# Performance work log

Measured on AMD Instinct MI355X. Metric: run time of the kernel, lower is better.

## Reference

```python
import jax, jax.numpy as jnp
import numpy as np

TOP_K = 2

def setup_inputs() -> dict:
    key = jax.random.key(0)
    ks = jax.random.split(key, 5)
    B, T, C, D, E = 2, 2048, 1024, 4096, 8
    init = 0.02  # typical GPT init scale
    return {
        "x": jax.random.normal(ks[0], (B, T, C), dtype=jnp.float32),
        "w_router": jax.random.normal(ks[1], (E, C), dtype=jnp.float32) * init,
        "w1": jax.random.normal(ks[2], (E, C, D), dtype=jnp.float32) * init,
        "b1": jnp.zeros((E, D), dtype=jnp.float32),
        "w2": jax.random.normal(ks[3], (E, D, C), dtype=jnp.float32) * init,
        "b2": jnp.zeros((E, C), dtype=jnp.float32),
    }

def reference(x, w_router, w1, b1, w2, b2):
    # Eval-mode MoE forward: no router noise, aux_loss = 0.
    B, T, C = x.shape
    E = w_router.shape[0]
    xf = x.reshape(B * T, C)                                   # [N, C]
    N = xf.shape[0]

    # Router: softmax over experts, top-2, renormalize.
    logits = jnp.einsum('nc,ec->ne', xf, w_router)             # [N, E]
    probs = jax.nn.softmax(logits, axis=-1)
    topw, topi = jax.lax.top_k(probs, TOP_K)                   # [N, K]
    topw = topw / jnp.sum(topw, axis=-1, keepdims=True)

    # Dense combine-weight matrix (scatter of top-k weights), zeros elsewhere.
    wdense = jnp.zeros((N, E), dtype=xf.dtype)
    wdense = wdense.at[jnp.arange(N)[:, None], topi].set(topw)  # [N, E]

    # Per-expert MLP (exact GELU, like torch nn.GELU default).
    h = jax.nn.gelu(jnp.einsum('nc,ecd->ned', xf, w1) + b1[None, :, :],
                    approximate=False)                          # [N, E, D]
    expert_out = jnp.einsum('ned,edc->nec', h, w2) + b2[None, :, :]  # [N, E, C]

    # Weighted scatter-combine: unselected experts have weight 0.
    out = jnp.einsum('ne,nec->nc', wdense, expert_out)          # [N, C]
    return out.reshape(B, T, C)
```

## Files before the change

### kernel.cpp

```cpp
#include <hip/hip_runtime.h>
#include <cstdint>

#define NTOK 4096
#define CDIM 1024
#define DDIM 4096
#define NEXP 8
#define PAIR_CAP 9216
#define MAXTILE 72

typedef __bf16 bf16x8 __attribute__((ext_vector_type(8)));
typedef float f32x4 __attribute__((ext_vector_type(4)));
typedef unsigned int u32x4 __attribute__((ext_vector_type(4)));
typedef unsigned short u16;

__device__ __forceinline__ u16 bf16_rne(float f) {
  unsigned u = __builtin_bit_cast(unsigned, f);
  u += 0x7fffu + ((u >> 16) & 1u);
  return (u16)(u >> 16);
}
__device__ __forceinline__ unsigned pk2(float a, float b) {
  return (unsigned)bf16_rne(a) | ((unsigned)bf16_rne(b) << 16);
}
__device__ __forceinline__ float bf2f(u16 v) {
  unsigned u = (unsigned)v << 16;
  return __builtin_bit_cast(float, u);
}
__device__ __forceinline__ bf16x8 ldfrag(const u16* p) {
  u32x4 v = *(const u32x4*)p;
  return __builtin_bit_cast(bf16x8, v);
}

typedef __attribute__((address_space(1))) const unsigned int as1_u32;
typedef __attribute__((address_space(3))) unsigned int as3_u32;
__device__ __forceinline__ void gload_lds16(const void* g, void* l) {
  __builtin_amdgcn_global_load_lds((as1_u32*)g, (as3_u32*)l, 16, 0, 0);
}

__global__ void k_router(const float* __restrict__ x, const float* __restrict__ wr,
                         int2* __restrict__ topi, float2* __restrict__ topw) {
  int n = blockIdx.x;
  int lane = threadIdx.x;
  const float* xr = x + (size_t)n * CDIM;
  float acc[NEXP];
#pragma unroll
  for (int e = 0; e < NEXP; ++e) acc[e] = 0.f;
  for (int c = lane; c < CDIM; c += 64) {
    float xv = xr[c];
#pragma unroll
    for (int e = 0; e < NEXP; ++e) acc[e] += xv * wr[e * CDIM + c];
  }
#pragma unroll
  for (int e = 0; e < NEXP; ++e) {
    float v = acc[e];
#pragma unroll
    for (int off = 32; off > 0; off >>= 1) v += __shfl_xor(v, off, 64);
    acc[e] = v;
  }
  if (lane == 0) {
    int i1 = 0; float l1 = acc[0];
#pragma unroll
    for (int e = 1; e < NEXP; ++e) if (acc[e] > l1) { l1 = acc[e]; i1 = e; }
    int i2 = (i1 == 0) ? 1 : 0; float l2 = acc[i2];
#pragma unroll
    for (int e = 0; e < NEXP; ++e)
      if (e != i1 && acc[e] > l2) { l2 = acc[e]; i2 = e; }
    float wa = 1.f / (1.f + expf(l2 - l1));
    topi[n] = make_int2(i1, i2);
    topw[n] = make_float2(wa, 1.f - wa);
  }
}

__global__ void k_count(const int2* __restrict__ topi, int* __restrict__ counts) {
  int n = blockIdx.x * blockDim.x + threadIdx.x;
  if (n < NTOK) {
    int2 tv = topi[n];
    atomicAdd(&counts[tv.x], 1);
    atomicAdd(&counts[tv.y], 1);
  }
}

__global__ void k_scan(const int* __restrict__ counts, int* __restrict__ poff,
                       int* __restrict__ cursor, int* __restrict__ ntiles,
                       int* __restrict__ tile_e, int* __restrict__ tile_base) {
  if (threadIdx.x == 0 && blockIdx.x == 0) {
    int o = 0, nt = 0;
    for (int e = 0; e < NEXP; ++e) {
      poff[e] = o;
      cursor[e] = o;
      int cap = (counts[e] + 127) & ~127;
      for (int tb = 0; tb < cap; tb += 128) { tile_e[nt] = e; tile_base[nt] = o + tb; ++nt; }
      o += cap;
    }
    poff[NEXP] = o;
    *ntiles = nt;
  }
}

__global__ void k_scatter(const int2* __restrict__ topi,
                          int* __restrict__ cursor, int* __restrict__ ptok,
                          int2* __restrict__ ppos) {
  int n = blockIdx.x * blockDim.x + threadIdx.x;
  if (n < NTOK) {
    int2 tv = topi[n];
    int p0 = atomicAdd(&cursor[tv.x], 1); ptok[p0] = n;
    int p1 = atomicAdd(&cursor[tv.y], 1); ptok[p1] = n;
    ppos[n] = make_int2(p0, p1);
  }
}

__global__ void k_xcast(const float* __restrict__ x, u16* __restrict__ xb) {
  int i = blockIdx.x * blockDim.x + threadIdx.x;
  float4 v = ((const float4*)x)[i];
  ushort4 o;
  o.x = bf16_rne(v.x); o.y = bf16_rne(v.y); o.z = bf16_rne(v.z); o.w = bf16_rne(v.w);
  ((ushort4*)xb)[i] = o;
}

__global__ __launch_bounds__(256) void k_transpose(const float* __restrict__ in,
                                                   u16* __restrict__ out, int K, int N) {
  __shared__ float tile[64][65];
  int e = blockIdx.z;
  int nb = blockIdx.x * 64, kb = blockIdx.y * 64;
  const float* src = in + (size_t)e * K * N + (size_t)kb * N + nb;
  int t = threadIdx.x;
#pragma unroll
  for (int j = 0; j < 4; ++j) {
    int idx4 = t + j * 256;
    int r = idx4 >> 4, c4 = idx4 & 15;
    float4 v = *(const float4*)&src[(size_t)r * N + c4 * 4];
    tile[r][c4 * 4 + 0] = v.x; tile[r][c4 * 4 + 1] = v.y;
    tile[r][c4 * 4 + 2] = v.z; tile[r][c4 * 4 + 3] = v.w;
  }
  __syncthreads();
  u16* dst = out + (size_t)e * N * K + (size_t)nb * K + kb;
#pragma unroll
  for (int j = 0; j < 8; ++j) {
    int idxp = t + j * 256;
    int n = idxp >> 5, kp = idxp & 31;
    unsigned pr = pk2(tile[kp * 2][n], tile[kp * 2 + 1][n]);
    *(unsigned*)&dst[(size_t)n * K + kp * 2] = pr;
  }
}

template <int KD, int NOUT, bool GATHER, bool DOGELU>
__global__ __launch_bounds__(256) void k_gemm(
    const u16* __restrict__ A, const u16* __restrict__ WT,
    const float* __restrict__ bias, const int* __restrict__ ntiles,
    const int* __restrict__ tile_e, const int* __restrict__ tile_base,
    const int* __restrict__ ptok, u16* __restrict__ Out) {
  int bx = blockIdx.x;
  if (bx >= *ntiles) return;
  int e = tile_e[bx];
  int pairbase = tile_base[bx];
  int colbase = blockIdx.y * 128;

  __shared__ __align__(16) u16 As[128 * 64];
  __shared__ __align__(16) u16 Bs[128 * 64];

  int t = threadIdx.x;
  int wid = t >> 6, lane = t & 63;
  int quad = lane >> 4, lm = lane & 15, l7 = lane & 7;
  int wm = wid & 1, wn = wid >> 1;
  int rl = lane >> 3, q = lane & 7;
  int kbl = (q - rl) & 7;

  const char* Ac = (const char*)A;
  const char* Wc = (const char*)WT;
  uint64_t gA[4], gB[4];
#pragma unroll
  for (int i = 0; i < 4; ++i) {
    int row = wid * 32 + i * 8 + rl;
    int arow = GATHER ? ptok[pairbase + row] : (pairbase + row);
    gA[i] = (uint64_t)arow * (KD * 2) + (uint64_t)kbl * 16;
    int brow = colbase + row;
    gB[i] = ((uint64_t)e * NOUT + brow) * (KD * 2) + (uint64_t)kbl * 16;
  }

  f32x4 acc[4][4];
  f32x4 zed = {0.f, 0.f, 0.f, 0.f};
#pragma unroll
  for (int a = 0; a < 4; ++a)
#pragma unroll
    for (int b = 0; b < 4; ++b) acc[a][b] = zed;

  for (int step = 0; step < KD / 64; ++step) {
    __syncthreads();
#pragma unroll
    for (int i = 0; i < 4; ++i)
      gload_lds16(Ac + gA[i] + (uint64_t)step * 128, (void*)&As[(wid * 32 + i * 8) * 64]);
#pragma unroll
    for (int i = 0; i < 4; ++i)
      gload_lds16(Wc + gB[i] + (uint64_t)step * 128, (void*)&Bs[(wid * 32 + i * 8) * 64]);
    __syncthreads();

#pragma unroll
    for (int s = 0; s < 2; ++s) {
      bf16x8 af[4], bfr[4];
#pragma unroll
      for (int tm = 0; tm < 4; ++tm) {
        int row = wm * 64 + tm * 16 + lm;
        int phys = (s * 4 + quad + l7) & 7;
        af[tm] = ldfrag(&As[row * 64 + phys * 8]);
      }
#pragma unroll
      for (int tn = 0; tn < 4; ++tn) {
        int col = wn * 64 + tn * 16 + lm;
        int phys = (s * 4 + quad + l7) & 7;
        bfr[tn] = ldfrag(&Bs[col * 64 + phys * 8]);
      }
#pragma unroll
      for (int tm = 0; tm < 4; ++tm)
#pragma unroll
        for (int tn = 0; tn < 4; ++tn)
          acc[tm][tn] = __builtin_amdgcn_mfma_f32_16x16x32_bf16(af[tm], bfr[tn], acc[tm][tn], 0, 0, 0);
    }
  }

#pragma unroll
  for (int tn = 0; tn < 4; ++tn) {
    int col = colbase + wn * 64 + tn * 16 + lm;
    float bv = bias[e * NOUT + col];
#pragma unroll
    for (int tm = 0; tm < 4; ++tm) {
      int row0 = pairbase + wm * 64 + tm * 16 + quad * 4;
#pragma unroll
      for (int i = 0; i < 4; ++i) {
        float vv = acc[tm][tn][i] + bv;
        if (DOGELU) vv = 0.5f * vv * (1.f + erff(vv * 0.70710678118654752f));
        Out[(size_t)(row0 + i) * NOUT + col] = bf16_rne(vv);
      }
    }
  }
}

__global__ __launch_bounds__(256) void k_combine(const u16* __restrict__ pairout,
                                                 const float2* __restrict__ topw,
                                                 const int2* __restrict__ ppos,
                                                 float* __restrict__ out) {
  int n = blockIdx.x, t = threadIdx.x;
  int2 p = ppos[n];
  float2 w = topw[n];
  ushort4 a = ((const ushort4*)(pairout + (size_t)p.x * CDIM))[t];
  ushort4 b = ((const ushort4*)(pairout + (size_t)p.y * CDIM))[t];
  float4 o;
  o.x = w.x * bf2f(a.x) + w.y * bf2f(b.x);
  o.y = w.x * bf2f(a.y) + w.y * bf2f(b.y);
  o.z = w.x * bf2f(a.z) + w.y * bf2f(b.z);
  o.w = w.x * bf2f(a.w) + w.y * bf2f(b.w);
  ((float4*)(out + (size_t)n * CDIM))[t] = o;
}

extern "C" void kernel_launch(void* const* d_in, const int* in_sizes, int n_in,
                              void* d_out, int out_size, void* d_ws, size_t ws_size,
                              hipStream_t stream) {
  const float* x  = (const float*)d_in[0];
  const float* wr = (const float*)d_in[1];
  const float* w1 = (const float*)d_in[2];
  const float* b1 = (const float*)d_in[3];
  const float* w2 = (const float*)d_in[4];
  const float* b2 = (const float*)d_in[5];
  float* out = (float*)d_out;
  char* ws = (char*)d_ws;

  int*    counts  = (int*)(ws + 0);
  int*    poff    = (int*)(ws + 64);
  int*    cursor  = (int*)(ws + 128);
  int*    ntiles  = (int*)(ws + 192);
  int*    tile_e  = (int*)(ws + 256);
  int*    tile_b  = (int*)(ws + 640);
  int2*   topi    = (int2*)(ws + 1024);
  float2* topw    = (float2*)(ws + 33792);
  int2*   ppos    = (int2*)(ws + 66560);
  int*    ptok    = (int*)(ws + 99328);
  u16*    xb      = (u16*)(ws + 136192);
  u16*    h       = (u16*)(ws + 8524800);
  u16*    wt      = (u16*)(ws + 84022272);
  u16*    pairout = (u16*)(ws + 151131136);

  hipMemsetAsync(ws, 0, 1024, stream);
  hipMemsetAsync(ws + 99328, 0, 36864, stream);

  k_router<<<NTOK, 64, 0, stream>>>(x, wr, topi, topw);
  k_count<<<NTOK / 256, 256, 0, stream>>>(topi, counts);
  k_scan<<<1, 64, 0, stream>>>(counts, poff, cursor, ntiles, tile_e, tile_b);
  k_scatter<<<NTOK / 256, 256, 0, stream>>>(topi, cursor, ptok, ppos);
  k_xcast<<<NTOK * CDIM / 4 / 256, 256, 0, stream>>>(x, xb);

  k_transpose<<<dim3(DDIM / 64, CDIM / 64, NEXP), 256, 0, stream>>>(w1, wt, CDIM, DDIM);
  k_gemm<CDIM, DDIM, true, true>
      <<<dim3(MAXTILE, DDIM / 128), 256, 0, stream>>>(xb, wt, b1, ntiles, tile_e, tile_b, ptok, h);

  k_transpose<<<dim3(CDIM / 64, DDIM / 64, NEXP), 256, 0, stream>>>(w2, wt, DDIM, CDIM);
  k_gemm<DDIM, CDIM, false, false>
      <<<dim3(MAXTILE, CDIM / 128), 256, 0, stream>>>(h, wt, b2, ntiles, tile_e, tile_b, ptok, pairout);

  k_combine<<<NTOK, 256, 0, stream>>>(pairout, topw, ppos, out);
}
```

Before: 695.1 us.

## Fuse prep kernels, split-K second GEMM, cheaper GELU, move b2 bias to combine

Router, x cast and both weight transposes are merged into one prep kernel, and count/scan/scatter into one single-block bucket kernel, to cut launch overhead and serialization. The second expert GEMM is split along K into two partial outputs, summed in the combine kernel when the workspace is large enough, to raise block-level parallelism. Exact erf GELU is replaced by a tanh-style sigmoid approximation, which adds small numeric error. The b2 bias is applied during the combine.

```diff
diff --git a/kernel.cpp b/kernel.cpp
--- a/kernel.cpp
+++ b/kernel.cpp
@@ -29,6 +29,10 @@
   u32x4 v = *(const u32x4*)p;
   return __builtin_bit_cast(bf16x8, v);
 }
+__device__ __forceinline__ float gelu_f(float v) {
+  float u = v + 0.044715f * v * v * v;
+  return v / (1.f + __expf(-1.5957691216f * u));
+}
 
 typedef __attribute__((address_space(1))) const unsigned int as1_u32;
 typedef __attribute__((address_space(3))) unsigned int as3_u32;
@@ -36,93 +40,10 @@
   __builtin_amdgcn_global_load_lds((as1_u32*)g, (as3_u32*)l, 16, 0, 0);
 }
 
-__global__ void k_router(const float* __restrict__ x, const float* __restrict__ wr,
-                         int2* __restrict__ topi, float2* __restrict__ topw) {
-  int n = blockIdx.x;
-  int lane = threadIdx.x;
-  const float* xr = x + (size_t)n * CDIM;
-  float acc[NEXP];
-#pragma unroll
-  for (int e = 0; e < NEXP; ++e) acc[e] = 0.f;
-  for (int c = lane; c < CDIM; c += 64) {
-    float xv = xr[c];
-#pragma unroll
-    for (int e = 0; e < NEXP; ++e) acc[e] += xv * wr[e * CDIM + c];
-  }
-#pragma unroll
-  for (int e = 0; e < NEXP; ++e) {
-    float v = acc[e];
-#pragma unroll
-    for (int off = 32; off > 0; off >>= 1) v += __shfl_xor(v, off, 64);
-    acc[e] = v;
-  }
-  if (lane == 0) {
-    int i1 = 0; float l1 = acc[0];
-#pragma unroll
-    for (int e = 1; e < NEXP; ++e) if (acc[e] > l1) { l1 = acc[e]; i1 = e; }
-    int i2 = (i1 == 0) ? 1 : 0; float l2 = acc[i2];
-#pragma unroll
-    for (int e = 0; e < NEXP; ++e)
-      if (e != i1 && acc[e] > l2) { l2 = acc[e]; i2 = e; }
-    float wa = 1.f / (1.f + expf(l2 - l1));
-    topi[n] = make_int2(i1, i2);
-    topw[n] = make_float2(wa, 1.f - wa);
-  }
-}
-
-__global__ void k_count(const int2* __restrict__ topi, int* __restrict__ counts) {
-  int n = blockIdx.x * blockDim.x + threadIdx.x;
-  if (n < NTOK) {
-    int2 tv = topi[n];
-    atomicAdd(&counts[tv.x], 1);
-    atomicAdd(&counts[tv.y], 1);
-  }
-}
-
-__global__ void k_scan(const int* __restrict__ counts, int* __restrict__ poff,
-                       int* __restrict__ cursor, int* __restrict__ ntiles,
-                       int* __restrict__ tile_e, int* __restrict__ tile_base) {
-  if (threadIdx.x == 0 && blockIdx.x == 0) {
-    int o = 0, nt = 0;
-    for (int e = 0; e < NEXP; ++e) {
-      poff[e] = o;
-      cursor[e] = o;
-      int cap = (counts[e] + 127) & ~127;
-      for (int tb = 0; tb < cap; tb += 128) { tile_e[nt] = e; tile_base[nt] = o + tb; ++nt; }
-      o += cap;
-    }
-    poff[NEXP] = o;
-    *ntiles = nt;
-  }
-}
-
-__global__ void k_scatter(const int2* __restrict__ topi,
-                          int* __restrict__ cursor, int* __restrict__ ptok,
-                          int2* __restrict__ ppos) {
-  int n = blockIdx.x * blockDim.x + threadIdx.x;
-  if (n < NTOK) {
-    int2 tv = topi[n];
-    int p0 = atomicAdd(&cursor[tv.x], 1); ptok[p0] = n;
-    int p1 = atomicAdd(&cursor[tv.y], 1); ptok[p1] = n;
-    ppos[n] = make_int2(p0, p1);
-  }
-}
-
-__global__ void k_xcast(const float* __restrict__ x, u16* __restrict__ xb) {
-  int i = blockIdx.x * blockDim.x + threadIdx.x;
-  float4 v = ((const float4*)x)[i];
-  ushort4 o;
-  o.x = bf16_rne(v.x); o.y = bf16_rne(v.y); o.z = bf16_rne(v.z); o.w = bf16_rne(v.w);
-  ((ushort4*)xb)[i] = o;
-}
-
-__global__ __launch_bounds__(256) void k_transpose(const float* __restrict__ in,
-                                                   u16* __restrict__ out, int K, int N) {
-  __shared__ float tile[64][65];
-  int e = blockIdx.z;
-  int nb = blockIdx.x * 64, kb = blockIdx.y * 64;
-  const float* src = in + (size_t)e * K * N + (size_t)kb * N + nb;
-  int t = threadIdx.x;
+__device__ __forceinline__ void transpose_tile(const float* __restrict__ src0,
+                                               u16* __restrict__ dst0, int K, int N,
+                                               int kb, int nb, int t, float tile[64][65]) {
+  const float* src = src0 + (size_t)kb * N + nb;
 #pragma unroll
   for (int j = 0; j < 4; ++j) {
     int idx4 = t + j * 256;
@@ -132,27 +53,132 @@
     tile[r][c4 * 4 + 2] = v.z; tile[r][c4 * 4 + 3] = v.w;
   }
   __syncthreads();
-  u16* dst = out + (size_t)e * N * K + (size_t)nb * K + kb;
+  u16* dst = dst0 + (size_t)nb * K + kb;
 #pragma unroll
   for (int j = 0; j < 8; ++j) {
     int idxp = t + j * 256;
     int n = idxp >> 5, kp = idxp & 31;
-    unsigned pr = pk2(tile[kp * 2][n], tile[kp * 2 + 1][n]);
-    *(unsigned*)&dst[(size_t)n * K + kp * 2] = pr;
-  }
-}
-
-template <int KD, int NOUT, bool GATHER, bool DOGELU>
+    *(unsigned*)&dst[(size_t)n * K + kp * 2] = pk2(tile[kp * 2][n], tile[kp * 2 + 1][n]);
+  }
+}
+
+#define RB 1024
+#define XB 4096
+#define TB 8192
+
+__global__ __launch_bounds__(256) void k_prep(
+    const float* __restrict__ x, const float* __restrict__ wr,
+    const float* __restrict__ w1, const float* __restrict__ w2,
+    int2* __restrict__ topi, float2* __restrict__ topw,
+    u16* __restrict__ xb, u16* __restrict__ wt1, u16* __restrict__ wt2) {
+  __shared__ float tile[64][65];
+  int b = blockIdx.x, t = threadIdx.x;
+  if (b < RB) {
+    int wid = t >> 6, lane = t & 63;
+    int n = b * 4 + wid;
+    const float* xr = x + (size_t)n * CDIM;
+    float acc[NEXP];
+#pragma unroll
+    for (int e = 0; e < NEXP; ++e) acc[e] = 0.f;
+    for (int c = lane; c < CDIM; c += 64) {
+      float xv = xr[c];
+#pragma unroll
+      for (int e = 0; e < NEXP; ++e) acc[e] += xv * wr[e * CDIM + c];
+    }
+#pragma unroll
+    for (int e = 0; e < NEXP; ++e) {
+      float v = acc[e];
+#pragma unroll
+      for (int off = 32; off > 0; off >>= 1) v += __shfl_xor(v, off, 64);
+      acc[e] = v;
+    }
+    if (lane == 0) {
+      int i1 = 0; float l1 = acc[0];
+#pragma unroll
+      for (int e = 1; e < NEXP; ++e) if (acc[e] > l1) { l1 = acc[e]; i1 = e; }
+      int i2 = (i1 == 0) ? 1 : 0; float l2 = acc[i2];
+#pragma unroll
+      for (int e = 0; e < NEXP; ++e)
+        if (e != i1 && acc[e] > l2) { l2 = acc[e]; i2 = e; }
+      float wa = 1.f / (1.f + __expf(l2 - l1));
+      topi[n] = make_int2(i1, i2);
+      topw[n] = make_float2(wa, 1.f - wa);
+    }
+  } else if (b < RB + XB) {
+    int i = (b - RB) * 256 + t;
+    float4 v = ((const float4*)x)[i];
+    ushort4 o;
+    o.x = bf16_rne(v.x); o.y = bf16_rne(v.y); o.z = bf16_rne(v.z); o.w = bf16_rne(v.w);
+    ((ushort4*)xb)[i] = o;
+  } else if (b < RB + XB + TB) {
+    int idx = b - (RB + XB);
+    int e = idx >> 10, rem = idx & 1023;
+    int nb = (rem & 63) * 64, kb = (rem >> 6) * 64;
+    transpose_tile(w1 + (size_t)e * CDIM * DDIM, wt1 + (size_t)e * DDIM * CDIM,
+                   CDIM, DDIM, kb, nb, t, tile);
+  } else {
+    int idx = b - (RB + XB + TB);
+    int e = idx >> 10, rem = idx & 1023;
+    int nb = (rem & 15) * 64, kb = (rem >> 4) * 64;
+    transpose_tile(w2 + (size_t)e * DDIM * CDIM, wt2 + (size_t)e * CDIM * DDIM,
+                   DDIM, CDIM, kb, nb, t, tile);
+  }
+}
+
+__global__ __launch_bounds__(256) void k_transpose_w2(const float* __restrict__ in,
+                                                      u16* __restrict__ out) {
+  __shared__ float tile[64][65];
+  int e = blockIdx.z;
+  transpose_tile(in + (size_t)e * DDIM * CDIM, out + (size_t)e * CDIM * DDIM,
+                 DDIM, CDIM, blockIdx.y * 64, blockIdx.x * 64, threadIdx.x, tile);
+}
+
+__global__ void k_bucket(const int2* __restrict__ topi, int* __restrict__ ptok,
+                         int2* __restrict__ ppos, int* __restrict__ ntiles,
+                         int* __restrict__ tile_e, int* __restrict__ tile_b) {
+  __shared__ int cnt[NEXP], cur[NEXP];
+  int t = threadIdx.x;
+  if (t < NEXP) cnt[t] = 0;
+  __syncthreads();
+  for (int n = t; n < NTOK; n += 1024) {
+    int2 tv = topi[n];
+    atomicAdd(&cnt[tv.x], 1);
+    atomicAdd(&cnt[tv.y], 1);
+  }
+  __syncthreads();
+  if (t == 0) {
+    int o = 0, nt = 0;
+    for (int e = 0; e < NEXP; ++e) {
+      cur[e] = o;
+      int cap = (cnt[e] + 127) & ~127;
+      for (int tb = 0; tb < cap; tb += 128) { tile_e[nt] = e; tile_b[nt] = o + tb; ++nt; }
+      o += cap;
+    }
+    *ntiles = nt;
+  }
+  __syncthreads();
+  for (int n = t; n < NTOK; n += 1024) {
+    int2 tv = topi[n];
+    int p0 = atomicAdd(&cur[tv.x], 1); ptok[p0] = n;
+    int p1 = atomicAdd(&cur[tv.y], 1); ptok[p1] = n;
+    ppos[n] = make_int2(p0, p1);
+  }
+}
+
+template <int KROW, int KLEN, int NOUT, bool GATHER, bool GELUBIAS, bool COLX>
 __global__ __launch_bounds__(256) void k_gemm(
     const u16* __restrict__ A, const u16* __restrict__ WT,
     const float* __restrict__ bias, const int* __restrict__ ntiles,
     const int* __restrict__ tile_e, const int* __restrict__ tile_base,
     const int* __restrict__ ptok, u16* __restrict__ Out) {
-  int bx = blockIdx.x;
-  if (bx >= *ntiles) return;
-  int e = tile_e[bx];
-  int pairbase = tile_base[bx];
-  int colbase = blockIdx.y * 128;
+  int tileIdx = COLX ? blockIdx.y : blockIdx.x;
+  int colIdx = COLX ? blockIdx.x : blockIdx.y;
+  if (tileIdx >= *ntiles) return;
+  int e = tile_e[tileIdx];
+  int pairbase = tile_base[tileIdx];
+  int colbase = colIdx * 128;
+  int kbase = blockIdx.z * KLEN;
+  u16* OutZ = Out + (size_t)blockIdx.z * ((size_t)PAIR_CAP * NOUT);
 
   __shared__ __align__(16) u16 As[128 * 64];
   __shared__ __align__(16) u16 Bs[128 * 64];
@@ -171,9 +197,9 @@
   for (int i = 0; i < 4; ++i) {
     int row = wid * 32 + i * 8 + rl;
     int arow = GATHER ? ptok[pairbase + row] : (pairbase + row);
-    gA[i] = (uint64_t)arow * (KD * 2) + (uint64_t)kbl * 16;
+    gA[i] = (uint64_t)arow * (KROW * 2) + (uint64_t)kbase * 2 + (uint64_t)kbl * 16;
     int brow = colbase + row;
-    gB[i] = ((uint64_t)e * NOUT + brow) * (KD * 2) + (uint64_t)kbl * 16;
+    gB[i] = ((uint64_t)e * NOUT + brow) * (KROW * 2) + (uint64_t)kbase * 2 + (uint64_t)kbl * 16;
   }
 
   f32x4 acc[4][4];
@@ -183,7 +209,7 @@
 #pragma unroll
     for (int b = 0; b < 4; ++b) acc[a][b] = zed;
 
-  for (int step = 0; step < KD / 64; ++step) {
+  for (int step = 0; step < KLEN / 64; ++step) {
     __syncthreads();
 #pragma unroll
     for (int i = 0; i < 4; ++i)
@@ -219,34 +245,47 @@
 #pragma unroll
   for (int tn = 0; tn < 4; ++tn) {
     int col = colbase + wn * 64 + tn * 16 + lm;
-    float bv = bias[e * NOUT + col];
+    float bv = 0.f;
+    if constexpr (GELUBIAS) bv = bias[e * NOUT + col];
 #pragma unroll
     for (int tm = 0; tm < 4; ++tm) {
       int row0 = pairbase + wm * 64 + tm * 16 + quad * 4;
 #pragma unroll
       for (int i = 0; i < 4; ++i) {
-        float vv = acc[tm][tn][i] + bv;
-        if (DOGELU) vv = 0.5f * vv * (1.f + erff(vv * 0.70710678118654752f));
-        Out[(size_t)(row0 + i) * NOUT + col] = bf16_rne(vv);
+        float vv = acc[tm][tn][i];
+        if constexpr (GELUBIAS) vv = gelu_f(vv + bv);
+        OutZ[(size_t)(row0 + i) * NOUT + col] = bf16_rne(vv);
       }
     }
   }
 }
 
-__global__ __launch_bounds__(256) void k_combine(const u16* __restrict__ pairout,
-                                                 const float2* __restrict__ topw,
-                                                 const int2* __restrict__ ppos,
-                                                 float* __restrict__ out) {
+__global__ __launch_bounds__(256) void k_combine(
+    const u16* __restrict__ P, const float2* __restrict__ topw,
+    const int2* __restrict__ ppos, const int2* __restrict__ topi,
+    const float* __restrict__ b2, float* __restrict__ out, int nparts) {
   int n = blockIdx.x, t = threadIdx.x;
   int2 p = ppos[n];
   float2 w = topw[n];
-  ushort4 a = ((const ushort4*)(pairout + (size_t)p.x * CDIM))[t];
-  ushort4 b = ((const ushort4*)(pairout + (size_t)p.y * CDIM))[t];
+  int2 ei = topi[n];
+  ushort4 a0 = ((const ushort4*)(P + (size_t)p.x * CDIM))[t];
+  ushort4 b0 = ((const ushort4*)(P + (size_t)p.y * CDIM))[t];
+  float ax = bf2f(a0.x), ay = bf2f(a0.y), az = bf2f(a0.z), aw = bf2f(a0.w);
+  float bx = bf2f(b0.x), by = bf2f(b0.y), bz = bf2f(b0.z), bw = bf2f(b0.w);
+  if (nparts == 2) {
+    const u16* P1 = P + (size_t)PAIR_CAP * CDIM;
+    ushort4 a1 = ((const ushort4*)(P1 + (size_t)p.x * CDIM))[t];
+    ushort4 b1v = ((const ushort4*)(P1 + (size_t)p.y * CDIM))[t];
+    ax += bf2f(a1.x); ay += bf2f(a1.y); az += bf2f(a1.z); aw += bf2f(a1.w);
+    bx += bf2f(b1v.x); by += bf2f(b1v.y); bz += bf2f(b1v.z); bw += bf2f(b1v.w);
+  }
+  float4 c0 = ((const float4*)(b2 + (size_t)ei.x * CDIM))[t];
+  float4 c1 = ((const float4*)(b2 + (size_t)ei.y * CDIM))[t];
   float4 o;
-  o.x = w.x * bf2f(a.x) + w.y * bf2f(b.x);
-  o.y = w.x * bf2f(a.y) + w.y * bf2f(b.y);
-  o.z = w.x * bf2f(a.z) + w.y * bf2f(b.z);
-  o.w = w.x * bf2f(a.w) + w.y * bf2f(b.w);
+  o.x = w.x * (ax + c0.x) + w.y * (bx + c1.x);
+  o.y = w.x * (ay + c0.y) + w.y * (by + c1.y);
+  o.z = w.x * (az + c0.z) + w.y * (bz + c1.z);
+  o.w = w.x * (aw + c0.w) + w.y * (bw + c1.w);
   ((float4*)(out + (size_t)n * CDIM))[t] = o;
 }
 
@@ -262,37 +301,42 @@
   float* out = (float*)d_out;
   char* ws = (char*)d_ws;
 
-  int*    counts  = (int*)(ws + 0);
-  int*    poff    = (int*)(ws + 64);
-  int*    cursor  = (int*)(ws + 128);
-  int*    ntiles  = (int*)(ws + 192);
-  int*    tile_e  = (int*)(ws + 256);
-  int*    tile_b  = (int*)(ws + 640);
-  int2*   topi    = (int2*)(ws + 1024);
-  float2* topw    = (float2*)(ws + 33792);
-  int2*   ppos    = (int2*)(ws + 66560);
-  int*    ptok    = (int*)(ws + 99328);
-  u16*    xb      = (u16*)(ws + 136192);
-  u16*    h       = (u16*)(ws + 8524800);
-  u16*    wt      = (u16*)(ws + 84022272);
-  u16*    pairout = (u16*)(ws + 151131136);
-
-  hipMemsetAsync(ws, 0, 1024, stream);
+  int*    ntiles = (int*)(ws + 192);
+  int*    tile_e = (int*)(ws + 256);
+  int*    tile_b = (int*)(ws + 640);
+  int2*   topi   = (int2*)(ws + 1024);
+  float2* topw   = (float2*)(ws + 33792);
+  int2*   ppos   = (int2*)(ws + 66560);
+  int*    ptok   = (int*)(ws + 99328);
+  u16*    xb     = (u16*)(ws + 136192);
+  u16*    h      = (u16*)(ws + 8524800);
+  u16*    wt1    = (u16*)(ws + 84022272);
+  u16*    wt2    = (u16*)(ws + 151131136);
+  u16*    parts  = (u16*)(ws + 84022272);
+  u16*    pairout= (u16*)(ws + 151131136);
+
+  bool big = ws_size >= 218240000ULL;
+
   hipMemsetAsync(ws + 99328, 0, 36864, stream);
 
-  k_router<<<NTOK, 64, 0, stream>>>(x, wr, topi, topw);
-  k_count<<<NTOK / 256, 256, 0, stream>>>(topi, counts);
-  k_scan<<<1, 64, 0, stream>>>(counts, poff, cursor, ntiles, tile_e, tile_b);
-  k_scatter<<<NTOK / 256, 256, 0, stream>>>(topi, cursor, ptok, ppos);
-  k_xcast<<<NTOK * CDIM / 4 / 256, 256, 0, stream>>>(x, xb);
-
-  k_transpose<<<dim3(DDIM / 64, CDIM / 64, NEXP), 256, 0, stream>>>(w1, wt, CDIM, DDIM);
-  k_gemm<CDIM, DDIM, true, true>
-      <<<dim3(MAXTILE, DDIM / 128), 256, 0, stream>>>(xb, wt, b1, ntiles, tile_e, tile_b, ptok, h);
-
-  k_transpose<<<dim3(CDIM / 64, DDIM / 64, NEXP), 256, 0, stream>>>(w2, wt, DDIM, CDIM);
-  k_gemm<DDIM, CDIM, false, false>
-      <<<dim3(MAXTILE, CDIM / 128), 256, 0, stream>>>(h, wt, b2, ntiles, tile_e, tile_b, ptok, pairout);
-
-  k_combine<<<NTOK, 256, 0, stream>>>(pairout, topw, ppos, out);
-}
+  k_prep<<<big ? (RB + XB + 2 * TB) : (RB + XB + TB), 256, 0, stream>>>(
+      x, wr, w1, w2, topi, topw, xb, wt1, wt2);
+  k_bucket<<<1, 1024, 0, stream>>>(topi, ptok, ppos, ntiles, tile_e, tile_b);
+
+  k_gemm<CDIM, CDIM, DDIM, true, true, false>
+      <<<dim3(MAXTILE, DDIM / 128, 1), 256, 0, stream>>>(
+          xb, wt1, b1, ntiles, tile_e, tile_b, ptok, h);
+
+  if (big) {
+    k_gemm<DDIM, DDIM / 2, CDIM, false, false, true>
+        <<<dim3(CDIM / 128, MAXTILE, 2), 256, 0, stream>>>(
+            h, wt2, nullptr, ntiles, tile_e, tile_b, ptok, parts);
+    k_combine<<<NTOK, 256, 0, stream>>>(parts, topw, ppos, topi, b2, out, 2);
+  } else {
+    k_transpose_w2<<<dim3(CDIM / 64, DDIM / 64, NEXP), 256, 0, stream>>>(w2, wt1);
+    k_gemm<DDIM, DDIM, CDIM, false, false, true>
+        <<<dim3(CDIM / 128, MAXTILE, 1), 256, 0, stream>>>(
+            h, wt1, nullptr, ntiles, tile_e, tile_b, ptok, pairout);
+    k_combine<<<NTOK, 256, 0, stream>>>(pairout, topw, ppos, topi, b2, out, 1);
+  }
+}
```

After: 577.4 us. 16.9% less time.
